# Optimization experiments

Hardware: AMD Instinct MI355X
Metric: run time of the kernel (lower is better)

## Reference

```python
import jax, jax.numpy as jnp
import numpy as np

N_HIDDEN = 4096
N_OUT = 128
BATCH = 512


def setup_inputs() -> dict:
    key = jax.random.key(0)
    k1, k2, k3, k4, k5 = jax.random.split(key, 5)
    H = jax.random.normal(k1, (BATCH, N_HIDDEN), dtype=jnp.float32)
    # p is the running inverse-covariance state; build it SPD-ish and well
    # scaled like a real OS-ELM state: p ~ (A A^T / n + reg*I)^-1-ish scale.
    A = jax.random.normal(k2, (N_HIDDEN, N_HIDDEN), dtype=jnp.float32)
    p = 0.001 * (A @ A.T) / N_HIDDEN + 0.01 * jnp.eye(N_HIDDEN, dtype=jnp.float32)
    beta = 0.02 * jax.random.normal(k3, (N_HIDDEN, N_OUT), dtype=jnp.float32)
    target = jax.random.normal(k4, (BATCH, N_OUT), dtype=jnp.float32)
    return {"H": H, "p": p, "beta": beta, "target": target}


def reference(H, p, beta, target):
    # Incremental OS-ELM recursive least-squares update (training branch,
    # after initial training is finished).
    B = H.shape[0]
    Hp = H @ p                              # [B, n]
    S = jnp.eye(B, dtype=H.dtype) + Hp @ H.T  # [B, B]
    temp = jnp.linalg.pinv(S)               # on-device pinv (TF used host np.linalg.pinv)
    pHT = p @ H.T                           # [n, B]
    p_new = p - (pHT @ temp) @ Hp           # [n, n]
    # beta update uses the updated p
    Hbeta = H @ beta                        # [B, o]
    beta_new = beta + (p_new @ H.T) @ (target - Hbeta)  # [n, o]
    out = H @ beta_new                      # [B, o]
    return out
```

## Files before the change

### kernel.cpp

```cpp
#include <hip/hip_runtime.h>
#include <hip/hip_bf16.h>


typedef __attribute__((ext_vector_type(8))) short short8;
typedef __attribute__((ext_vector_type(4))) float f32x4;

#define NH 4096
#define NO 128
#define NBATCH 512

__device__ __forceinline__ unsigned short f2b(float x) {
  return __builtin_bit_cast(unsigned short, __float2bfloat16(x));
}

__device__ __forceinline__ float bu2f(unsigned short u) {
  return __builtin_bit_cast(float, ((unsigned int)u) << 16);
}

__device__ __forceinline__ float b2f_lo(unsigned int u) {
  return __builtin_bit_cast(float, u << 16);
}
__device__ __forceinline__ float b2f_hi(unsigned int u) {
  return __builtin_bit_cast(float, u & 0xffff0000u);
}

__device__ __forceinline__ void gload_lds16(const void* g, void* l) {
  __builtin_amdgcn_global_load_lds(
      (const __attribute__((address_space(1))) unsigned int*)g,
      (__attribute__((address_space(3))) unsigned int*)l, 16, 0, 0);
}

__global__ __launch_bounds__(256) void k_cast(const float* __restrict__ src,
                                              unsigned short* __restrict__ dst) {
  int i = blockIdx.x * 256 + threadIdx.x;
  float4 v = reinterpret_cast<const float4*>(src)[i];
  ushort4 o;
  o.x = f2b(v.x); o.y = f2b(v.y); o.z = f2b(v.z); o.w = f2b(v.w);
  reinterpret_cast<ushort4*>(dst)[i] = o;
}

__global__ __launch_bounds__(256) void k_cast_bt(const float* __restrict__ beta,
                                                 unsigned short* __restrict__ bT) {
  __shared__ unsigned short tile[128][130];
  const int t = threadIdx.x;
  const int k0 = blockIdx.x * 128;
  {
    const int r = t >> 1, c0 = (t & 1) * 64;
    const float* src = &beta[(size_t)(k0 + r) * NO + c0];
    #pragma unroll
    for (int i = 0; i < 16; ++i) {
      float4 v = *(const float4*)(src + i * 4);
      tile[r][c0 + i * 4 + 0] = f2b(v.x);
      tile[r][c0 + i * 4 + 1] = f2b(v.y);
      tile[r][c0 + i * 4 + 2] = f2b(v.z);
      tile[r][c0 + i * 4 + 3] = f2b(v.w);
    }
  }
  __syncthreads();
  {
    const int c = t >> 1, h = (t & 1) * 64;
    unsigned short* dst = &bT[(size_t)c * NH + k0 + h];
    #pragma unroll
    for (int i = 0; i < 16; ++i) {
      ushort4 o;
      o.x = tile[h + i * 4 + 0][c];
      o.y = tile[h + i * 4 + 1][c];
      o.z = tile[h + i * 4 + 2][c];
      o.w = tile[h + i * 4 + 3][c];
      *(ushort4*)(dst + i * 4) = o;
    }
  }
}

__global__ __launch_bounds__(512, 2) void k_gemm_hp(
    const unsigned short* __restrict__ A,
    const float* __restrict__ P,
    unsigned short* __restrict__ Cp) {
  __shared__ __align__(16) unsigned short As[2][128 * 64];
  __shared__ __align__(16) unsigned short Bs[2][128 * 64];
  const int t = threadIdx.x, w = t >> 6, l = t & 63;
  const int n0 = blockIdx.x * 128, m0 = blockIdx.y * 128;
  const int kb = blockIdx.z * 1024;
  const int wr = w >> 2, wc = w & 3;
  const int fl = l & 15, fk = (l >> 4) * 8;
  const int srow = l >> 3;
  const int kcolsw = (((l & 7) ^ srow) * 8);
  const unsigned short* asrc0 = A + (size_t)(m0 + w * 16 + srow) * NH + kb + kcolsw;
  const unsigned short* asrc1 = A + (size_t)(m0 + w * 16 + 8 + srow) * NH + kb + kcolsw;
  const int brow = t >> 3, bg = t & 7;
  const float* bsrc0 = P + (size_t)(n0 + brow) * NH + kb + bg * 8;
  const float* bsrc1 = P + (size_t)(n0 + 64 + brow) * NH + kb + bg * 8;
  const int bx = (bg ^ (brow & 7)) * 8;
  const int bwoff0 = brow * 64 + bx;
  const int bwoff1 = bwoff0 + 64 * 64;

  f32x4 z = {0.f, 0.f, 0.f, 0.f};
  f32x4 acc00 = z, acc01 = z, acc10 = z, acc11 = z;
  f32x4 acc20 = z, acc21 = z, acc30 = z, acc31 = z;

  const int xr = (fl & 7) * 8;

#define STAGE_A(kt, buf)                                    \
  {                                                         \
    const int kn = (kt) * 64;                               \
    gload_lds16(asrc0 + kn, &As[(buf)][w * 1024]);          \
    gload_lds16(asrc1 + kn, &As[(buf)][w * 1024 + 512]);    \
  }

#define LOAD_B(kt, r0, r1, r2, r3)                          \
  {                                                         \
    const float* b0p = bsrc0 + (kt) * 64;                   \
    const float* b1p = bsrc1 + (kt) * 64;                   \
    r0 = *(const float4*)b0p;  r1 = *(const float4*)(b0p + 4); \
    r2 = *(const float4*)b1p;  r3 = *(const float4*)(b1p + 4); \
  }

#define WRITE_B(buf, r0, r1, r2, r3)                        \
  {                                                         \
    short8 p0, p1;                                          \
    p0[0] = (short)f2b(r0.x); p0[1] = (short)f2b(r0.y);     \
    p0[2] = (short)f2b(r0.z); p0[3] = (short)f2b(r0.w);     \
    p0[4] = (short)f2b(r1.x); p0[5] = (short)f2b(r1.y);     \
    p0[6] = (short)f2b(r1.z); p0[7] = (short)f2b(r1.w);     \
    p1[0] = (short)f2b(r2.x); p1[1] = (short)f2b(r2.y);     \
    p1[2] = (short)f2b(r2.z); p1[3] = (short)f2b(r2.w);     \
    p1[4] = (short)f2b(r3.x); p1[5] = (short)f2b(r3.y);     \
    p1[6] = (short)f2b(r3.z); p1[7] = (short)f2b(r3.w);     \
    *(short8*)&Bs[(buf)][bwoff0] = p0;                      \
    *(short8*)&Bs[(buf)][bwoff1] = p1;                      \
  }

#define COMPUTE_HP(buf)                                                        \
  {                                                                            \
    const unsigned short* Ab = As[(buf)];                                      \
    const unsigned short* Bb = Bs[(buf)];                                      \
    _Pragma("unroll")                                                          \
    for (int ks = 0; ks < 2; ++ks) {                                           \
      const int x = (ks * 32 + fk) ^ xr;                                       \
      short8 b0 = *(const short8*)&Bb[(wc * 32 + fl) * 64 + x];                \
      short8 b1 = *(const short8*)&Bb[(wc * 32 + 16 + fl) * 64 + x];           \
      short8 a0 = *(const short8*)&Ab[(wr * 64 + fl) * 64 + x];                \
      short8 a1 = *(const short8*)&Ab[(wr * 64 + 16 + fl) * 64 + x];           \
      short8 a2 = *(const short8*)&Ab[(wr * 64 + 32 + fl) * 64 + x];           \
      short8 a3 = *(const short8*)&Ab[(wr * 64 + 48 + fl) * 64 + x];           \
      acc00 = __builtin_amdgcn_mfma_f32_16x16x32_bf16(a0, b0, acc00, 0, 0, 0); \
      acc01 = __builtin_amdgcn_mfma_f32_16x16x32_bf16(a0, b1, acc01, 0, 0, 0); \
      acc10 = __builtin_amdgcn_mfma_f32_16x16x32_bf16(a1, b0, acc10, 0, 0, 0); \
      acc11 = __builtin_amdgcn_mfma_f32_16x16x32_bf16(a1, b1, acc11, 0, 0, 0); \
      acc20 = __builtin_amdgcn_mfma_f32_16x16x32_bf16(a2, b0, acc20, 0, 0, 0); \
      acc21 = __builtin_amdgcn_mfma_f32_16x16x32_bf16(a2, b1, acc21, 0, 0, 0); \
      acc30 = __builtin_amdgcn_mfma_f32_16x16x32_bf16(a3, b0, acc30, 0, 0, 0); \
      acc31 = __builtin_amdgcn_mfma_f32_16x16x32_bf16(a3, b1, acc31, 0, 0, 0); \
    }                                                                          \
  }

  float4 e0, e1, e2, e3, o0, o1, o2, o3;
  LOAD_B(0, e0, e1, e2, e3);
  STAGE_A(0, 0);
  LOAD_B(1, o0, o1, o2, o3);
  asm volatile("s_waitcnt vmcnt(6)" ::: "memory");
  WRITE_B(0, e0, e1, e2, e3);

  for (int k2 = 0; k2 < 14; k2 += 2) {
    asm volatile("s_waitcnt vmcnt(4) lgkmcnt(0)" ::: "memory");
    __builtin_amdgcn_s_barrier();
    STAGE_A(k2 + 1, 1);
    asm volatile("s_waitcnt vmcnt(2)" ::: "memory");
    WRITE_B(1, o0, o1, o2, o3);
    LOAD_B(k2 + 2, e0, e1, e2, e3);
    COMPUTE_HP(0);
    asm volatile("s_waitcnt vmcnt(4) lgkmcnt(0)" ::: "memory");
    __builtin_amdgcn_s_barrier();
    STAGE_A(k2 + 2, 0);
    asm volatile("s_waitcnt vmcnt(2)" ::: "memory");
    WRITE_B(0, e0, e1, e2, e3);
    LOAD_B(k2 + 3, o0, o1, o2, o3);
    COMPUTE_HP(1);
  }
  asm volatile("s_waitcnt vmcnt(4) lgkmcnt(0)" ::: "memory");
  __builtin_amdgcn_s_barrier();
  STAGE_A(15, 1);
  asm volatile("s_waitcnt vmcnt(2)" ::: "memory");
  WRITE_B(1, o0, o1, o2, o3);
  COMPUTE_HP(0);
  asm volatile("s_waitcnt vmcnt(0) lgkmcnt(0)" ::: "memory");
  __builtin_amdgcn_s_barrier();
  COMPUTE_HP(1);
#undef COMPUTE_HP
#undef WRITE_B
#undef LOAD_B
#undef STAGE_A

  unsigned short* Co = Cp + (size_t)blockIdx.z * (NBATCH * NH);
  const int rb = (l >> 4) * 4;
  const int cw = n0 + wc * 32 + fl;
  #pragma unroll
  for (int j = 0; j < 4; ++j) {
    int m = m0 + wr * 64 + rb + j;
    Co[(size_t)m * NH + cw]        = f2b(acc00[j]);
    Co[(size_t)m * NH + cw + 16]   = f2b(acc01[j]);
    Co[(size_t)(m + 16) * NH + cw]      = f2b(acc10[j]);
    Co[(size_t)(m + 16) * NH + cw + 16] = f2b(acc11[j]);
    Co[(size_t)(m + 32) * NH + cw]      = f2b(acc20[j]);
    Co[(size_t)(m + 32) * NH + cw + 16] = f2b(acc21[j]);
    Co[(size_t)(m + 48) * NH + cw]      = f2b(acc30[j]);
    Co[(size_t)(m + 48) * NH + cw + 16] = f2b(acc31[j]);
  }
}

__global__ __launch_bounds__(256) void k_reduce_hp(const unsigned short* __restrict__ Hpp,
                                                   unsigned short* __restrict__ Hp) {
  int i = blockIdx.x * 256 + threadIdx.x;
  const int stride = NBATCH * NH / 4;
  ushort4 a = reinterpret_cast<const ushort4*>(Hpp)[i];
  ushort4 b = reinterpret_cast<const ushort4*>(Hpp)[i + stride];
  ushort4 c = reinterpret_cast<const ushort4*>(Hpp)[i + 2 * stride];
  ushort4 d = reinterpret_cast<const ushort4*>(Hpp)[i + 3 * stride];
  ushort4 o;
  o.x = f2b((bu2f(a.x) + bu2f(b.x)) + (bu2f(c.x) + bu2f(d.x)));
  o.y = f2b((bu2f(a.y) + bu2f(b.y)) + (bu2f(c.y) + bu2f(d.y)));
  o.z = f2b((bu2f(a.z) + bu2f(b.z)) + (bu2f(c.z) + bu2f(d.z)));
  o.w = f2b((bu2f(a.w) + bu2f(b.w)) + (bu2f(c.w) + bu2f(d.w)));
  reinterpret_cast<ushort4*>(Hp)[i] = o;
}

__global__ __launch_bounds__(512, 2) void k_gemm_s(
    const unsigned short* __restrict__ A,
    const unsigned short* __restrict__ Bm,
    float* __restrict__ Spart) {
  __shared__ __align__(16) unsigned short As[3][128 * 64];
  __shared__ __align__(16) unsigned short Bs[3][64 * 64];
  const int t = threadIdx.x, w = t >> 6, l = t & 63;
  const int m0 = blockIdx.y * 128, n0 = blockIdx.x * 64;
  const int kb = blockIdx.z * 512;
  const int wr = w >> 1, wc = w & 1, fl = l & 15, fk = (l >> 4) * 8;
  const int srow = l >> 3;
  const int kcolsw = (((l & 7) ^ srow) * 8);
  const unsigned short* asrc0 = A + (size_t)(m0 + w * 16 + srow) * NH + kb + kcolsw;
  const unsigned short* asrc1 = A + (size_t)(m0 + w * 16 + 8 + srow) * NH + kb + kcolsw;
  const unsigned short* bsrc  = Bm + (size_t)(n0 + w * 8 + srow) * NH + kb + kcolsw;

  f32x4 z = {0.f, 0.f, 0.f, 0.f};
  f32x4 acc00 = z, acc01 = z, acc10 = z, acc11 = z;

  const int xr = (fl & 7) * 8;

#define STAGE_S(kt, buf)                                    \
  {                                                         \
    const int kn = (kt) * 64;                               \
    gload_lds16(asrc0 + kn, &As[(buf)][w * 1024]);          \
    gload_lds16(asrc1 + kn, &As[(buf)][w * 1024 + 512]);    \
    gload_lds16(bsrc + kn,  &Bs[(buf)][w * 512]);           \
  }

#define COMPUTE_S(buf)                                                         \
  {                                                                            \
    const unsigned short* Ab = As[(buf)];                                      \
    const unsigned short* Bb = Bs[(buf)];                                      \
    _Pragma("unroll")                                                          \
    for (int ks = 0; ks < 2; ++ks) {                                           \
      const int x = (ks * 32 + fk) ^ xr;                                       \
      short8 a0 = *(const short8*)&Ab[(wr * 32 + fl) * 64 + x];                \
      short8 a1 = *(const short8*)&Ab[(wr * 32 + 16 + fl) * 64 + x];           \
      short8 b0 = *(const short8*)&Bb[(wc * 32 + fl) * 64 + x];                \
      short8 b1 = *(const short8*)&Bb[(wc * 32 + 16 + fl) * 64 + x];           \
      acc00 = __builtin_amdgcn_mfma_f32_16x16x32_bf16(a0, b0, acc00, 0, 0, 0); \
      acc01 = __builtin_amdgcn_mfma_f32_16x16x32_bf16(a0, b1, acc01, 0, 0, 0); \
      acc10 = __builtin_amdgcn_mfma_f32_16x16x32_bf16(a1, b0, acc10, 0, 0, 0); \
      acc11 = __builtin_amdgcn_mfma_f32_16x16x32_bf16(a1, b1, acc11, 0, 0, 0); \
    }                                                                          \
  }

#define ITER_S(kt, buf)                                           \
  {                                                               \
    asm volatile("s_waitcnt vmcnt(3) lgkmcnt(0)" ::: "memory");   \
    __builtin_amdgcn_s_barrier();                                 \
    if ((kt) + 2 < 8) STAGE_S((kt) + 2, ((buf) + 2) % 3);         \
    COMPUTE_S(buf);                                               \
  }

  STAGE_S(0, 0);
  STAGE_S(1, 1);
  ITER_S(0, 0); ITER_S(1, 1); ITER_S(2, 2);
  ITER_S(3, 0); ITER_S(4, 1); ITER_S(5, 2);
  ITER_S(6, 0);
  asm volatile("s_waitcnt vmcnt(0) lgkmcnt(0)" ::: "memory");
  __builtin_amdgcn_s_barrier();
  COMPUTE_S(1);
#undef ITER_S
#undef COMPUTE_S
#undef STAGE_S

  float* sp = Spart + (size_t)blockIdx.z * (512 * 512);
  const int rb = (l >> 4) * 4;
  #pragma unroll
  for (int j = 0; j < 4; ++j) {
    int m = m0 + wr * 32 + rb + j;
    sp[(size_t)m * 512 + n0 + wc * 32 + fl]      = acc00[j];
    sp[(size_t)m * 512 + n0 + wc * 32 + 16 + fl] = acc01[j];
    int m2 = m + 16;
    sp[(size_t)m2 * 512 + n0 + wc * 32 + fl]      = acc10[j];
    sp[(size_t)m2 * 512 + n0 + wc * 32 + 16 + fl] = acc11[j];
  }
}

__global__ __launch_bounds__(512, 2) void k_r_gemm(
    const unsigned short* __restrict__ A,
    const unsigned short* __restrict__ Bm,
    float* __restrict__ rpart) {
  __shared__ __align__(16) unsigned short As[2][128 * 64];
  __shared__ __align__(16) unsigned short Bs[2][64 * 64];
  const int t = threadIdx.x, w = t >> 6, l = t & 63;
  const int m0 = blockIdx.y * 128, n0 = blockIdx.x * 64;
  const int kb = blockIdx.z * 256;
  const int wr = w >> 1, wc = w & 1, fl = l & 15, fk = (l >> 4) * 8;
  const int srow = l >> 3, kcol = (l & 7) * 8;
  const unsigned short* asrc0 = A + (size_t)(m0 + w * 16 + srow) * NH + kb + kcol;
  const unsigned short* asrc1 = A + (size_t)(m0 + w * 16 + 8 + srow) * NH + kb + kcol;
  const unsigned short* bsrc  = Bm + (size_t)(n0 + w * 8 + srow) * NH + kb + kcol;

  f32x4 z = {0.f, 0.f, 0.f, 0.f};
  f32x4 acc00 = z, acc01 = z, acc10 = z, acc11 = z;

  gload_lds16(asrc0, &As[0][w * 1024]);
  gload_lds16(asrc1, &As[0][w * 1024 + 512]);
  gload_lds16(bsrc,  &Bs[0][w * 512]);
  __syncthreads();

  int cur = 0;
  for (int kt = 0; kt < 4; ++kt) {
    if (kt + 1 < 4) {
      const int kn = (kt + 1) * 64;
      gload_lds16(asrc0 + kn, &As[cur ^ 1][w * 1024]);
      gload_lds16(asrc1 + kn, &As[cur ^ 1][w * 1024 + 512]);
      gload_lds16(bsrc  + kn, &Bs[cur ^ 1][w * 512]);
    }
    const unsigned short* Ab = As[cur];
    const unsigned short* Bb = Bs[cur];
    #pragma unroll
    for (int ks = 0; ks < 2; ++ks) {
      short8 a0 = *(const short8*)&Ab[(wr * 32 + fl) * 64 + ks * 32 + fk];
      short8 a1 = *(const short8*)&Ab[(wr * 32 + 16 + fl) * 64 + ks * 32 + fk];
      short8 b0 = *(const short8*)&Bb[(wc * 32 + fl) * 64 + ks * 32 + fk];
      short8 b1 = *(const short8*)&Bb[(wc * 32 + 16 + fl) * 64 + ks * 32 + fk];
      acc00 = __builtin_amdgcn_mfma_f32_16x16x32_bf16(a0, b0, acc00, 0, 0, 0);
      acc01 = __builtin_amdgcn_mfma_f32_16x16x32_bf16(a0, b1, acc01, 0, 0, 0);
      acc10 = __builtin_amdgcn_mfma_f32_16x16x32_bf16(a1, b0, acc10, 0, 0, 0);
      acc11 = __builtin_amdgcn_mfma_f32_16x16x32_bf16(a1, b1, acc11, 0, 0, 0);
    }
    __syncthreads();
    cur ^= 1;
  }

  float* rp = rpart + (size_t)blockIdx.z * (NBATCH * NO);
  const int rb = (l >> 4) * 4;
  #pragma unroll
  for (int j = 0; j < 4; ++j) {
    int m = m0 + wr * 32 + rb + j;
    rp[(size_t)m * NO + n0 + wc * 32 + fl]      = acc00[j];
    rp[(size_t)m * NO + n0 + wc * 32 + 16 + fl] = acc01[j];
    int m2 = m + 16;
    rp[(size_t)m2 * NO + n0 + wc * 32 + fl]      = acc10[j];
    rp[(size_t)m2 * NO + n0 + wc * 32 + 16 + fl] = acc11[j];
  }
}

__global__ __launch_bounds__(256) void k_reduce_s(const float* __restrict__ Spart,
                                                  unsigned short* __restrict__ Sb) {
  int i = blockIdx.x * 256 + threadIdx.x;
  float acc = ((i >> 9) == (i & 511)) ? 1.0f : 0.0f;
  #pragma unroll
  for (int c = 0; c < 8; ++c) acc += Spart[c * 262144 + i];
  Sb[i] = f2b(acc);
}

__global__ __launch_bounds__(256) void k_r_reduce16(const float* __restrict__ rpart,
                                                    const float* __restrict__ target,
                                                    float* __restrict__ rbuf) {
  int i = blockIdx.x * 256 + threadIdx.x;
  float acc = target[i];
  #pragma unroll
  for (int c = 0; c < 16; ++c) acc -= rpart[c * (NBATCH * NO) + i];
  rbuf[i] = acc;
}

__device__ __forceinline__ float block_reduce1(float a, float* red) {
  #pragma unroll
  for (int off = 32; off; off >>= 1) a += __shfl_xor(a, off);
  const int t = threadIdx.x;
  __syncthreads();
  if ((t & 63) == 0) red[t >> 6] = a;
  __syncthreads();
  float ra = 0.f;
  #pragma unroll
  for (int q2 = 0; q2 < 8; ++q2) ra += red[q2];
  return ra;
}

#define CG_ITERS 6
__global__ __launch_bounds__(512) void k_cg(const unsigned short* __restrict__ Sb,
                                            const float* __restrict__ rbuf,
                                            const float* __restrict__ target,
                                            float* __restrict__ out) {
  __shared__ float pl[512];
  __shared__ float vred[8][512];
  __shared__ float red[8];
  const int t = threadIdx.x;
  const int q = t >> 6;
  const int rt = t & 63;
  const int j = blockIdx.x;

  float r = rbuf[(size_t)t * NO + j];
  float x = 0.f;
  pl[t] = r;
  float rho = block_reduce1(r * r, red);
  __syncthreads();

  const uint4* S8 = (const uint4*)Sb;
  const uint4* sp = S8 + (size_t)(q * 64) * 64 + rt;
  const float* pq = &pl[q * 64];

  for (int it = 0; it < CG_ITERS; ++it) {
    float a0 = 0.f, a1 = 0.f, a2 = 0.f, a3 = 0.f;
    float a4 = 0.f, a5 = 0.f, a6 = 0.f, a7 = 0.f;
    #pragma unroll 8
    for (int k = 0; k < 64; ++k) {
      uint4 sv = sp[(size_t)k * 64];
      float p = pq[k];
      a0 += b2f_lo(sv.x) * p; a1 += b2f_hi(sv.x) * p;
      a2 += b2f_lo(sv.y) * p; a3 += b2f_hi(sv.y) * p;
      a4 += b2f_lo(sv.z) * p; a5 += b2f_hi(sv.z) * p;
      a6 += b2f_lo(sv.w) * p; a7 += b2f_hi(sv.w) * p;
    }
    *(float4*)&vred[q][8 * rt]     = make_float4(a0, a1, a2, a3);
    *(float4*)&vred[q][8 * rt + 4] = make_float4(a4, a5, a6, a7);
    __syncthreads();
    float v = 0.f;
    #pragma unroll
    for (int c = 0; c < 8; ++c) v += vred[c][t];
    float p = pl[t];
    float ppv = block_reduce1(p * v, red);
    float al = rho / ppv;
    x += al * p;
    r -= al * v;
    float rhon = block_reduce1(r * r, red);
    float be = rhon / rho;
    rho = rhon;
    __syncthreads();
    pl[t] = r + be * p;
    __syncthreads();
  }
  out[(size_t)t * NO + j] = target[(size_t)t * NO + j] - x;
}

extern "C" void kernel_launch(void* const* d_in, const int* in_sizes, int n_in,
                              void* d_out, int out_size, void* d_ws, size_t ws_size,
                              hipStream_t stream) {
  (void)in_sizes; (void)n_in; (void)out_size; (void)ws_size;
  const float* H      = (const float*)d_in[0];
  const float* P      = (const float*)d_in[1];
  const float* beta   = (const float*)d_in[2];
  const float* target = (const float*)d_in[3];
  float* out = (float*)d_out;

  char* ws = (char*)d_ws;
  unsigned short* Hb  = (unsigned short*)(ws);
  unsigned short* Hp  = (unsigned short*)(ws + (4u << 20));
  unsigned short* Hpp = (unsigned short*)(ws + (8u << 20));
  float* Spart        = (float*)(ws + (8u << 20));
  unsigned short* bT  = (unsigned short*)(ws + (16u << 20));
  float* rpart        = (float*)(ws + (17u << 20));
  unsigned short* Sb  = (unsigned short*)(ws + (21u << 20));
  float* rbuf         = (float*)(ws + (21u << 20) + (512u << 10));

  k_cast<<<2048, 256, 0, stream>>>(H, Hb);
  k_gemm_hp<<<dim3(32, 4, 4), 512, 0, stream>>>(Hb, P, Hpp);
  k_reduce_hp<<<2048, 256, 0, stream>>>(Hpp, Hp);
  k_gemm_s<<<dim3(8, 4, 8), 512, 0, stream>>>(Hp, Hb, Spart);
  k_reduce_s<<<1024, 256, 0, stream>>>(Spart, Sb);
  k_cast_bt<<<32, 256, 0, stream>>>(beta, bT);
  k_r_gemm<<<dim3(2, 4, 16), 512, 0, stream>>>(Hb, bT, rpart);
  k_r_reduce16<<<256, 256, 0, stream>>>(rpart, target, rbuf);
  k_cg<<<NO, 512, 0, stream>>>(Sb, rbuf, target, out);
}
```

Baseline: 99.60 us.

## Deepen H@P register prefetch to three B stages and raise occupancy hint

Restructures the H@P GEMM main loop so the fp32 P tiles are prefetched into registers two iterations ahead, rotating through three register sets instead of two. Inserts sched_barriers so STAGE_A issue order is kept, and the loop is unrolled by six. Launch bounds now target four blocks per CU instead of two. The aim is to hide global-load latency on P. The cost is extra register pressure from the third buffer, which conflicts with the higher occupancy target and may cause spills.

```diff
diff --git a/kernel.cpp b/kernel.cpp
--- a/kernel.cpp
+++ b/kernel.cpp
@@ -72,7 +72,7 @@
   }
 }
 
-__global__ __launch_bounds__(512, 2) void k_gemm_hp(
+__global__ __launch_bounds__(512, 4) void k_gemm_hp(
     const unsigned short* __restrict__ A,
     const float* __restrict__ P,
     unsigned short* __restrict__ Cp) {
@@ -154,38 +154,47 @@
     }                                                                          \
   }
 
-  float4 e0, e1, e2, e3, o0, o1, o2, o3;
+#define ITER_HP(kt, ab, c0, c1, c2, c3, d0, d1, d2, d3, DL)       \
+  {                                                               \
+    asm volatile("s_waitcnt vmcnt(4) lgkmcnt(0)" ::: "memory");   \
+    __builtin_amdgcn_s_barrier();                                 \
+    STAGE_A((kt) + 1, (ab) ^ 1);                                  \
+    __builtin_amdgcn_sched_barrier(0);                            \
+    WRITE_B((ab) ^ 1, c0, c1, c2, c3);                            \
+    if (DL) LOAD_B((kt) + 3, d0, d1, d2, d3);                     \
+    COMPUTE_HP(ab);                                               \
+  }
+
+  float4 e0, e1, e2, e3, o0, o1, o2, o3, u0, u1, u2, u3;
   LOAD_B(0, e0, e1, e2, e3);
   STAGE_A(0, 0);
+  __builtin_amdgcn_sched_barrier(0);
   LOAD_B(1, o0, o1, o2, o3);
   asm volatile("s_waitcnt vmcnt(6)" ::: "memory");
   WRITE_B(0, e0, e1, e2, e3);
-
-  for (int k2 = 0; k2 < 14; k2 += 2) {
-    asm volatile("s_waitcnt vmcnt(4) lgkmcnt(0)" ::: "memory");
+  LOAD_B(2, u0, u1, u2, u3);
+
+  for (int k6 = 0; k6 < 12; k6 += 6) {
+    ITER_HP(k6 + 0, 0, o0, o1, o2, o3, e0, e1, e2, e3, 1);
+    ITER_HP(k6 + 1, 1, u0, u1, u2, u3, o0, o1, o2, o3, 1);
+    ITER_HP(k6 + 2, 0, e0, e1, e2, e3, u0, u1, u2, u3, 1);
+    ITER_HP(k6 + 3, 1, o0, o1, o2, o3, e0, e1, e2, e3, 1);
+    ITER_HP(k6 + 4, 0, u0, u1, u2, u3, o0, o1, o2, o3, 1);
+    ITER_HP(k6 + 5, 1, e0, e1, e2, e3, u0, u1, u2, u3, 1);
+  }
+  ITER_HP(12, 0, o0, o1, o2, o3, e0, e1, e2, e3, 1);
+  ITER_HP(13, 1, u0, u1, u2, u3, o0, o1, o2, o3, 0);
+  {
+    asm volatile("s_waitcnt vmcnt(0) lgkmcnt(0)" ::: "memory");
     __builtin_amdgcn_s_barrier();
-    STAGE_A(k2 + 1, 1);
-    asm volatile("s_waitcnt vmcnt(2)" ::: "memory");
-    WRITE_B(1, o0, o1, o2, o3);
-    LOAD_B(k2 + 2, e0, e1, e2, e3);
+    STAGE_A(15, 1);
+    WRITE_B(1, e0, e1, e2, e3);
     COMPUTE_HP(0);
-    asm volatile("s_waitcnt vmcnt(4) lgkmcnt(0)" ::: "memory");
-    __builtin_amdgcn_s_barrier();
-    STAGE_A(k2 + 2, 0);
-    asm volatile("s_waitcnt vmcnt(2)" ::: "memory");
-    WRITE_B(0, e0, e1, e2, e3);
-    LOAD_B(k2 + 3, o0, o1, o2, o3);
-    COMPUTE_HP(1);
-  }
-  asm volatile("s_waitcnt vmcnt(4) lgkmcnt(0)" ::: "memory");
-  __builtin_amdgcn_s_barrier();
-  STAGE_A(15, 1);
-  asm volatile("s_waitcnt vmcnt(2)" ::: "memory");
-  WRITE_B(1, o0, o1, o2, o3);
-  COMPUTE_HP(0);
+  }
   asm volatile("s_waitcnt vmcnt(0) lgkmcnt(0)" ::: "memory");
   __builtin_amdgcn_s_barrier();
   COMPUTE_HP(1);
+#undef ITER_HP
 #undef COMPUTE_HP
 #undef WRITE_B
 #undef LOAD_B
```

After: 100.5 us. About the same (+0.9%).
